# Kernel tuning notes

Hardware: AMD Instinct MI355X
Metric: run time of the kernel (lower is better)

## Reference

```python
import jax, jax.numpy as jnp
import numpy as np


def setup_inputs() -> dict:
    key = jax.random.key(0)
    k1, k2, k3, k4 = jax.random.split(key, 4)
    B, T, d_model, d_internal = 4, 2048, 1024, 64
    x = jax.random.normal(k1, (B, T, d_model), dtype=jnp.float32)
    # torch.nn.Linear weights: [out_features, in_features]
    s = 1.0 / np.sqrt(d_model)
    W_Q = jax.random.uniform(k2, (d_internal, d_model), jnp.float32, -s, s)
    W_K = jax.random.uniform(k3, (d_internal, d_model), jnp.float32, -s, s)
    W_V = jax.random.uniform(k4, (d_internal, d_model), jnp.float32, -s, s)
    return {"x": x, "W_Q": W_Q, "W_K": W_K, "W_V": W_V}


def reference(x, W_Q, W_K, W_V):
    B, T, C = x.shape  # C == d_model
    Q = jnp.einsum('btc,dc->btd', x, W_Q)
    K = jnp.einsum('btc,dc->btd', x, W_K)
    # Faithful to source bug: V is computed with W_K, W_V is unused.
    V = jnp.einsum('btc,dc->btd', x, W_K)
    scale = C ** (-0.5)  # source scales by d_model, not d_internal
    attn = jnp.einsum('btd,bsd->bts', Q, K) * scale  # [B,T,T]
    causal = jnp.tril(jnp.ones((T, T), dtype=bool))
    attn = jnp.where(causal[None, :, :], attn, -jnp.inf)
    attn = jax.nn.softmax(attn, axis=-1)
    return jnp.einsum('bts,bsd->btd', attn, V)
```

## Files before the change

### kernel.cpp

```cpp
#include <hip/hip_runtime.h>
#include <hip/hip_bf16.h>
#include <cstdint>
#include <cstddef>

#define BB 4
#define TT 2048
#define DM 1024
#define DH 64

typedef __attribute__((ext_vector_type(8))) short short8;
typedef __attribute__((ext_vector_type(4))) float floatx4;

__device__ __forceinline__ unsigned short f2bf(float f) {
    union { float f; unsigned int u; } v; v.f = f;
    unsigned int u = v.u;
    u += 0x7fffu + ((u >> 16) & 1u);
    return (unsigned short)(u >> 16);
}

__device__ __forceinline__ short8 cvt8(float4 lo, float4 hi) {
    short8 r;
    r[0] = (short)f2bf(lo.x); r[1] = (short)f2bf(lo.y);
    r[2] = (short)f2bf(lo.z); r[3] = (short)f2bf(lo.w);
    r[4] = (short)f2bf(hi.x); r[5] = (short)f2bf(hi.y);
    r[6] = (short)f2bf(hi.z); r[7] = (short)f2bf(hi.w);
    return r;
}

#define WTHREADS (8 * 32 * 64)

__global__ __launch_bounds__(256) void wtile_kernel(const float* __restrict__ wq,
                                                    const float* __restrict__ wk,
                                                    unsigned short* __restrict__ wbt) {
    const int j  = blockIdx.x * 256 + threadIdx.x;
    const int l  = j & 63;
    const int kc = (j >> 6) & 31;
    const int nt = j >> 11;
    const float* wbase = (nt < 4) ? wq : wk;
    const float* src = wbase + (size_t)((nt & 3) * 16 + (l & 15)) * DM
                             + kc * 32 + (l >> 4) * 8;
    float4 a = *reinterpret_cast<const float4*>(src);
    float4 b = *reinterpret_cast<const float4*>(src + 4);
    *reinterpret_cast<short8*>(wbt + (size_t)j * 8) = cvt8(a, b);
}

__global__ __launch_bounds__(256) void proj_kernel(const float* __restrict__ x,
                                                   const unsigned short* __restrict__ wbt,
                                                   unsigned short* __restrict__ qo,
                                                   unsigned short* __restrict__ ko,
                                                   unsigned short* __restrict__ kt) {
    __shared__ __align__(16) unsigned short sA[2][16 * 64 * 8];

    const int tid  = threadIdx.x;
    const int wave = tid >> 6;
    const int lane = tid & 63;
    const int col  = lane & 15;
    const int quad = lane >> 4;
    const int mt   = blockIdx.x;

    const float* xtile = x + (size_t)mt * 16 * DM;
    const unsigned short* bq = wbt + ((size_t)wave * 32 * 64) * 8;
    const unsigned short* bk = wbt + ((size_t)(4 + wave) * 32 * 64) * 8;

    floatx4 accQ = (floatx4){0.f, 0.f, 0.f, 0.f};
    floatx4 accK = (floatx4){0.f, 0.f, 0.f, 0.f};

#pragma unroll 4
    for (int i = 0; i < 4; ++i) {
        const int e  = tid + i * 256;
        const int kc = e >> 6;
        const int l  = e & 63;
        const float* src = xtile + (size_t)(l & 15) * DM + kc * 32 + (l >> 4) * 8;
        float4 a = *reinterpret_cast<const float4*>(src);
        float4 b = *reinterpret_cast<const float4*>(src + 4);
        *reinterpret_cast<short8*>(sA[0] + (size_t)e * 8) = cvt8(a, b);
    }
    __syncthreads();

    float4 h1a[4], h1b[4];
#pragma unroll 4
    for (int i = 0; i < 4; ++i) {
        const int e  = tid + i * 256;
        const int kc = 16 + (e >> 6);
        const int l  = e & 63;
        const float* src = xtile + (size_t)(l & 15) * DM + kc * 32 + (l >> 4) * 8;
        h1a[i] = *reinterpret_cast<const float4*>(src);
        h1b[i] = *reinterpret_cast<const float4*>(src + 4);
    }

#pragma unroll
    for (int kc = 0; kc < 16; ++kc) {
        short8 a  = *reinterpret_cast<const short8*>(sA[0] + ((size_t)kc * 64 + lane) * 8);
        short8 b0 = *reinterpret_cast<const short8*>(bq + ((size_t)kc * 64 + lane) * 8);
        short8 b1 = *reinterpret_cast<const short8*>(bk + ((size_t)kc * 64 + lane) * 8);
        accQ = __builtin_amdgcn_mfma_f32_16x16x32_bf16(a, b0, accQ, 0, 0, 0);
        accK = __builtin_amdgcn_mfma_f32_16x16x32_bf16(a, b1, accK, 0, 0, 0);
    }

#pragma unroll 4
    for (int i = 0; i < 4; ++i) {
        const int e = tid + i * 256;
        *reinterpret_cast<short8*>(sA[1] + (size_t)e * 8) = cvt8(h1a[i], h1b[i]);
    }
    __syncthreads();

#pragma unroll
    for (int kc = 0; kc < 16; ++kc) {
        short8 a  = *reinterpret_cast<const short8*>(sA[1] + ((size_t)kc * 64 + lane) * 8);
        short8 b0 = *reinterpret_cast<const short8*>(bq + ((size_t)(16 + kc) * 64 + lane) * 8);
        short8 b1 = *reinterpret_cast<const short8*>(bk + ((size_t)(16 + kc) * 64 + lane) * 8);
        accQ = __builtin_amdgcn_mfma_f32_16x16x32_bf16(a, b0, accQ, 0, 0, 0);
        accK = __builtin_amdgcn_mfma_f32_16x16x32_bf16(a, b1, accK, 0, 0, 0);
    }

    const int g = wave * 16 + col;
    unsigned short hk[4];
#pragma unroll
    for (int r = 0; r < 4; ++r) {
        const size_t row = (size_t)(mt * 16 + quad * 4 + r);
        qo[row * DH + g] = f2bf(accQ[r] * 0.03125f);
        hk[r] = f2bf(accK[r]);
        ko[row * DH + g] = hk[r];
    }

    __syncthreads();
    unsigned short* kts = (unsigned short*)sA;
#pragma unroll
    for (int r = 0; r < 4; ++r)
        kts[g * 16 + quad * 4 + r] = hk[r];
    __syncthreads();
    if (tid < 128) {
        const int d  = tid >> 1;
        const int s8 = (tid & 1) * 8;
        const int b4 = mt >> 7;
        const int s0 = (mt & 127) * 16 + s8;
        short8 v = *reinterpret_cast<const short8*>(kts + d * 16 + s8);
        *reinterpret_cast<short8*>(kt + ((size_t)(b4 * 64 + d)) * TT + s0) = v;
    }
}

__global__ __launch_bounds__(128) void flash1_kernel(const unsigned short* __restrict__ qb,
                                                     const unsigned short* __restrict__ kb,
                                                     const unsigned short* __restrict__ ktb,
                                                     float* __restrict__ Op,
                                                     float* __restrict__ ml) {
    const int c  = blockIdx.x & 15;
    const int qt = (blockIdx.x >> 4) & 63;
    const int b  = blockIdx.x >> 10;
    if (4 * c > qt) return;

    __shared__ __align__(16) unsigned short Pl[2][4][16][40];

    const int tid  = threadIdx.x;
    const int wave = tid >> 6;
    const int lane = tid & 63;
    const int col  = lane & 15;
    const int quad = lane >> 4;

    const int q0    = qt * 32;
    const int qrow  = q0 + wave * 16;
    const int s_beg = c * 128;
    const int s_end = min(s_beg + 128, q0 + 32);

    const unsigned short* qp  = qb  + ((size_t)b * TT + qrow) * DH;
    const unsigned short* kp  = kb  + (size_t)b * TT * DH;
    const unsigned short* ktp = ktb + (size_t)b * 64 * TT;

    short8 qf0 = *reinterpret_cast<const short8*>(qp + (size_t)col * DH + quad * 8);
    short8 qf1 = *reinterpret_cast<const short8*>(qp + (size_t)col * DH + 32 + quad * 8);

    floatx4 o[4];
#pragma unroll
    for (int t = 0; t < 4; ++t) o[t] = (floatx4){0.f, 0.f, 0.f, 0.f};
    float lrow[4] = {0.f, 0.f, 0.f, 0.f};
    int   myq[4];
#pragma unroll
    for (int r = 0; r < 4; ++r) myq[r] = qrow + quad * 4 + r;
    const float LOG2E = 1.44269504f;

    auto body = [&](int s0, int slot, bool domask) {
        float sv[2][4];
#pragma unroll
        for (int st = 0; st < 2; ++st) {
            const unsigned short* kr = kp + (size_t)(s0 + st * 16 + col) * DH + quad * 8;
            short8 kf0 = *reinterpret_cast<const short8*>(kr);
            short8 kf1 = *reinterpret_cast<const short8*>(kr + 32);
            floatx4 z = (floatx4){0.f, 0.f, 0.f, 0.f};
            z = __builtin_amdgcn_mfma_f32_16x16x32_bf16(qf0, kf0, z, 0, 0, 0);
            z = __builtin_amdgcn_mfma_f32_16x16x32_bf16(qf1, kf1, z, 0, 0, 0);
            const int skey = s0 + st * 16 + col;
#pragma unroll
            for (int r = 0; r < 4; ++r) {
                float p = __builtin_exp2f(z[r] * LOG2E);
                if (domask) p = (skey <= myq[r]) ? p : 0.f;
                sv[st][r] = p;
                lrow[r] += p;
            }
        }
#pragma unroll
        for (int st = 0; st < 2; ++st)
#pragma unroll
            for (int r = 0; r < 4; ++r)
                Pl[wave][slot][quad * 4 + r][st * 16 + col] = f2bf(sv[st][r]);
        short8 pf = *reinterpret_cast<const short8*>(&Pl[wave][slot][col][quad * 8]);

#pragma unroll
        for (int t = 0; t < 4; ++t) {
            short8 vf = *reinterpret_cast<const short8*>(
                ktp + (size_t)(t * 16 + col) * TT + s0 + quad * 8);
            o[t] = __builtin_amdgcn_mfma_f32_16x16x32_bf16(pf, vf, o[t], 0, 0, 0);
        }
    };

    const int nIter = (s_end - s_beg) >> 5;
    if (nIter == 4) {
        body(s_beg,      0, false);
        body(s_beg + 32, 1, false);
        body(s_beg + 64, 2, false);
        body(s_beg + 96, 3, q0 == s_beg + 96);
    } else {
        for (int i = 0; i < nIter; ++i) {
            const int s0 = s_beg + 32 * i;
            body(s0, i & 3, s0 == q0);
        }
    }

#pragma unroll
    for (int m = 1; m < 16; m <<= 1)
#pragma unroll
        for (int r = 0; r < 4; ++r)
            lrow[r] += __shfl_xor(lrow[r], m, 64);

    const int slot = (b * 64 + qt) * 16 + c;
    float* op = Op + (size_t)slot * 2048;
#pragma unroll
    for (int t = 0; t < 4; ++t)
#pragma unroll
        for (int r = 0; r < 4; ++r)
            op[(size_t)(wave * 16 + quad * 4 + r) * DH + t * 16 + col] = o[t][r];
    if (col == 0) {
        float* mlp = ml + (size_t)slot * 32;
#pragma unroll
        for (int r = 0; r < 4; ++r)
            mlp[wave * 16 + quad * 4 + r] = lrow[r];
    }
}

__global__ __launch_bounds__(256) void merge_kernel(const float* __restrict__ Op,
                                                    const float* __restrict__ ml,
                                                    float* __restrict__ out) {
    const int qt  = blockIdx.x & 63;
    const int b   = blockIdx.x >> 6;
    const int nch = (qt >> 2) + 1;
    const int t   = threadIdx.x;
    const int row = t >> 3;
    const int c8  = (t & 7) * 8;
    const size_t base = (size_t)blockIdx.x * 16;

    float L = 0.f;
    float a[8];
#pragma unroll
    for (int i = 0; i < 8; ++i) a[i] = 0.f;
#pragma unroll 4
    for (int c = 0; c < nch; ++c) {
        L += ml[(base + c) * 32 + row];
        const float* op = Op + (base + c) * 2048 + (size_t)row * 64 + c8;
        float4 v0 = *reinterpret_cast<const float4*>(op);
        float4 v1 = *reinterpret_cast<const float4*>(op + 4);
        a[0] += v0.x; a[1] += v0.y; a[2] += v0.z; a[3] += v0.w;
        a[4] += v1.x; a[5] += v1.y; a[6] += v1.z; a[7] += v1.w;
    }
    const float inv = 1.0f / L;
    float* o = out + ((size_t)b * TT + qt * 32 + row) * DH + c8;
    float4 r0 = {a[0] * inv, a[1] * inv, a[2] * inv, a[3] * inv};
    float4 r1 = {a[4] * inv, a[5] * inv, a[6] * inv, a[7] * inv};
    *reinterpret_cast<float4*>(o)     = r0;
    *reinterpret_cast<float4*>(o + 4) = r1;
}

extern "C" void kernel_launch(void* const* d_in, const int* in_sizes, int n_in,
                              void* d_out, int out_size, void* d_ws, size_t ws_size,
                              hipStream_t stream) {
    const float* x  = (const float*)d_in[0];
    const float* wq = (const float*)d_in[1];
    const float* wk = (const float*)d_in[2];

    unsigned short* wbt = (unsigned short*)d_ws;
    unsigned short* qo  = wbt + (size_t)WTHREADS * 8;
    unsigned short* ko  = qo + (size_t)BB * TT * DH;
    unsigned short* kt  = ko + (size_t)BB * TT * DH;
    float* Op = (float*)(kt + (size_t)BB * DH * TT);
    float* ml = Op + (size_t)4096 * 2048;
    float* out = (float*)d_out;

    hipLaunchKernelGGL(wtile_kernel,  dim3(WTHREADS / 256), dim3(256), 0, stream, wq, wk, wbt);
    hipLaunchKernelGGL(proj_kernel,   dim3((BB * TT) / 16), dim3(256), 0, stream, x, wbt, qo, ko, kt);
    hipLaunchKernelGGL(flash1_kernel, dim3(BB * 64 * 16),   dim3(128), 0, stream, qo, ko, kt, Op, ml);
    hipLaunchKernelGGL(merge_kernel,  dim3(BB * 64),        dim3(256), 0, stream, Op, ml, out);
}
```

Measured before the change: 127.2 us.

## Fuse split-KV merge into flash kernel via last-block atomic counter, store partials in bf16

Removes the separate merge kernel. Each flash block now increments a per-(batch, query-tile) atomic counter, and the last block to finish sums the partial outputs and row sums and writes the normalized result. Partial outputs are stored as bf16 instead of fp32, halving their write and read traffic. This saves a kernel launch and reduces memory traffic, at the cost of extra rounding error in the partials plus threadfence and atomic overhead. Counters are zeroed in the weight-tiling kernel.

New measurement: 456.0 us. +258.6%, slower.

```diff
diff --git a/kernel.cpp b/kernel.cpp
--- a/kernel.cpp
+++ b/kernel.cpp
@@ -16,6 +16,12 @@
     unsigned int u = v.u;
     u += 0x7fffu + ((u >> 16) & 1u);
     return (unsigned short)(u >> 16);
+}
+
+__device__ __forceinline__ float bf2f(unsigned short h) {
+    union { unsigned int u; float f; } v;
+    v.u = ((unsigned int)h) << 16;
+    return v.f;
 }
 
 __device__ __forceinline__ short8 cvt8(float4 lo, float4 hi) {
@@ -31,7 +37,9 @@
 
 __global__ __launch_bounds__(256) void wtile_kernel(const float* __restrict__ wq,
                                                     const float* __restrict__ wk,
-                                                    unsigned short* __restrict__ wbt) {
+                                                    unsigned short* __restrict__ wbt,
+                                                    int* __restrict__ cnt) {
+    if (blockIdx.x == 0) cnt[threadIdx.x] = 0;
     const int j  = blockIdx.x * 256 + threadIdx.x;
     const int l  = j & 63;
     const int kc = (j >> 6) & 31;
@@ -142,14 +150,17 @@
 __global__ __launch_bounds__(128) void flash1_kernel(const unsigned short* __restrict__ qb,
                                                      const unsigned short* __restrict__ kb,
                                                      const unsigned short* __restrict__ ktb,
-                                                     float* __restrict__ Op,
-                                                     float* __restrict__ ml) {
+                                                     unsigned short* __restrict__ Opb,
+                                                     float* __restrict__ ml,
+                                                     int* __restrict__ cnt,
+                                                     float* __restrict__ out) {
     const int c  = blockIdx.x & 15;
     const int qt = (blockIdx.x >> 4) & 63;
     const int b  = blockIdx.x >> 10;
     if (4 * c > qt) return;
 
     __shared__ __align__(16) unsigned short Pl[2][4][16][40];
+    __shared__ int sLast;
 
     const int tid  = threadIdx.x;
     const int wave = tid >> 6;
@@ -231,51 +242,55 @@
         for (int r = 0; r < 4; ++r)
             lrow[r] += __shfl_xor(lrow[r], m, 64);
 
-    const int slot = (b * 64 + qt) * 16 + c;
-    float* op = Op + (size_t)slot * 2048;
+    const int pair = (b << 6) + qt;
+    const int slot = pair * 16 + c;
+    unsigned short* op = Opb + (size_t)slot * 2048;
 #pragma unroll
     for (int t = 0; t < 4; ++t)
 #pragma unroll
         for (int r = 0; r < 4; ++r)
-            op[(size_t)(wave * 16 + quad * 4 + r) * DH + t * 16 + col] = o[t][r];
+            op[(size_t)(wave * 16 + quad * 4 + r) * DH + t * 16 + col] = f2bf(o[t][r]);
     if (col == 0) {
         float* mlp = ml + (size_t)slot * 32;
 #pragma unroll
         for (int r = 0; r < 4; ++r)
             mlp[wave * 16 + quad * 4 + r] = lrow[r];
     }
-}
-
-__global__ __launch_bounds__(256) void merge_kernel(const float* __restrict__ Op,
-                                                    const float* __restrict__ ml,
-                                                    float* __restrict__ out) {
-    const int qt  = blockIdx.x & 63;
-    const int b   = blockIdx.x >> 6;
-    const int nch = (qt >> 2) + 1;
-    const int t   = threadIdx.x;
-    const int row = t >> 3;
-    const int c8  = (t & 7) * 8;
-    const size_t base = (size_t)blockIdx.x * 16;
-
+
+    const int nvalid = (qt >> 2) + 1;
+    __threadfence();
+    if (tid == 0)
+        sLast = (atomicAdd(&cnt[pair], 1) == nvalid - 1) ? 1 : 0;
+    __syncthreads();
+    if (!sLast) return;
+    __threadfence();
+
+    const int row = tid >> 2;
+    const int cg  = (tid & 3) * 16;
+    float acc[16];
+#pragma unroll
+    for (int i = 0; i < 16; ++i) acc[i] = 0.f;
     float L = 0.f;
-    float a[8];
-#pragma unroll
-    for (int i = 0; i < 8; ++i) a[i] = 0.f;
 #pragma unroll 4
-    for (int c = 0; c < nch; ++c) {
-        L += ml[(base + c) * 32 + row];
-        const float* op = Op + (base + c) * 2048 + (size_t)row * 64 + c8;
-        float4 v0 = *reinterpret_cast<const float4*>(op);
-        float4 v1 = *reinterpret_cast<const float4*>(op + 4);
-        a[0] += v0.x; a[1] += v0.y; a[2] += v0.z; a[3] += v0.w;
-        a[4] += v1.x; a[5] += v1.y; a[6] += v1.z; a[7] += v1.w;
+    for (int cc = 0; cc < nvalid; ++cc) {
+        const size_t sbase = (size_t)pair * 16 + cc;
+        L += ml[sbase * 32 + row];
+        const unsigned short* p = Opb + sbase * 2048 + (size_t)row * 64 + cg;
+        short8 v0 = *reinterpret_cast<const short8*>(p);
+        short8 v1 = *reinterpret_cast<const short8*>(p + 8);
+#pragma unroll
+        for (int j = 0; j < 8; ++j) {
+            acc[j]     += bf2f((unsigned short)v0[j]);
+            acc[8 + j] += bf2f((unsigned short)v1[j]);
+        }
     }
     const float inv = 1.0f / L;
-    float* o = out + ((size_t)b * TT + qt * 32 + row) * DH + c8;
-    float4 r0 = {a[0] * inv, a[1] * inv, a[2] * inv, a[3] * inv};
-    float4 r1 = {a[4] * inv, a[5] * inv, a[6] * inv, a[7] * inv};
-    *reinterpret_cast<float4*>(o)     = r0;
-    *reinterpret_cast<float4*>(o + 4) = r1;
+    float* od = out + ((size_t)b * TT + q0 + row) * DH + cg;
+#pragma unroll
+    for (int i = 0; i < 4; ++i) {
+        float4 v = {acc[i*4] * inv, acc[i*4+1] * inv, acc[i*4+2] * inv, acc[i*4+3] * inv};
+        *reinterpret_cast<float4*>(od + i * 4) = v;
+    }
 }
 
 extern "C" void kernel_launch(void* const* d_in, const int* in_sizes, int n_in,
@@ -289,12 +304,13 @@
     unsigned short* qo  = wbt + (size_t)WTHREADS * 8;
     unsigned short* ko  = qo + (size_t)BB * TT * DH;
     unsigned short* kt  = ko + (size_t)BB * TT * DH;
-    float* Op = (float*)(kt + (size_t)BB * DH * TT);
-    float* ml = Op + (size_t)4096 * 2048;
+    unsigned short* Opb = kt + (size_t)BB * DH * TT;
+    float* ml  = (float*)(Opb + (size_t)4096 * 2048);
+    int*   cnt = (int*)(ml + (size_t)4096 * 32);
     float* out = (float*)d_out;
 
-    hipLaunchKernelGGL(wtile_kernel,  dim3(WTHREADS / 256), dim3(256), 0, stream, wq, wk, wbt);
+    hipLaunchKernelGGL(wtile_kernel,  dim3(WTHREADS / 256), dim3(256), 0, stream, wq, wk, wbt, cnt);
     hipLaunchKernelGGL(proj_kernel,   dim3((BB * TT) / 16), dim3(256), 0, stream, x, wbt, qo, ko, kt);
-    hipLaunchKernelGGL(flash1_kernel, dim3(BB * 64 * 16),   dim3(128), 0, stream, qo, ko, kt, Op, ml);
-    hipLaunchKernelGGL(merge_kernel,  dim3(BB * 64),        dim3(256), 0, stream, Op, ml, out);
-}
+    hipLaunchKernelGGL(flash1_kernel, dim3(BB * 64 * 16),   dim3(128), 0, stream,
+                       qo, ko, kt, Opb, ml, cnt, out);
+}
```
